# Performance work log

Measured on AMD Instinct MI355X. Metric: run time of the kernel, lower is better.

## Reference

```python
import jax, jax.numpy as jnp
import numpy as np

TOKENS = 8192
MODEL_DIM = 4096
PROMPT_DIM = 64
NUM_EXPERTS = 8
TOP_K = 2
EPS = float(np.finfo(np.float32).eps)


def setup_inputs() -> dict:
    key = jax.random.key(0)
    k1, k2, k3 = jax.random.split(key, 3)
    x = jax.random.normal(k1, (TOKENS, MODEL_DIM), dtype=jnp.float32)
    prompt = jax.random.normal(k2, (TOKENS, PROMPT_DIM), dtype=jnp.float32)
    # gate linear: Linear(model_dim + prompt_dim, num_experts, bias=True)
    W = jax.random.normal(k3, (MODEL_DIM + PROMPT_DIM, NUM_EXPERTS), dtype=jnp.float32) * 0.02
    b = jnp.zeros((NUM_EXPERTS,), dtype=jnp.float32)
    return {"x": x, "prompt": prompt, "W": W, "b": b}


def reference(x, prompt, W, b):
    # eval path: no jitter, no noise (self.training is False)
    logits = jnp.concatenate([x, prompt], axis=-1) @ W + b          # [T, E]
    _, topk_idx = jax.lax.top_k(logits, TOP_K)                      # [T, K]
    masks = jax.nn.one_hot(topk_idx, NUM_EXPERTS, dtype=jnp.float32)  # [T, K, E]
    gates = jax.nn.softmax(logits, axis=-1)                         # [T, E]
    gates_s = jnp.einsum("te,tke->tk", gates, masks)               # masked gather-sum
    if TOP_K > 1:
        denom = jnp.maximum(gates_s.sum(axis=-1, keepdims=True), EPS)
        gates_s = gates_s / denom
    # masks[:, i] == masks_se[i], gates_s[:, i] == gates_s[i] in the torch code
    return masks, gates_s
```

## Files before the change

### kernel.cpp

```cpp
#include <hip/hip_runtime.h>
#include <math.h>

#define NE 8
#define KDIM 4096
#define PDIM 64
#define WROWS (KDIM + PDIM)
#define EPS_F32 1.1920929e-07f
#define NCHUNK 16
#define DEPTH 3

typedef float f4 __attribute__((ext_vector_type(4)));

__global__ __launch_bounds__(256)
void transpose_w(const float* __restrict__ W, float* __restrict__ Wt) {
    const int k = blockIdx.x * 256 + threadIdx.x;
    if (k < WROWS) {
        float v[NE];
#pragma unroll
        for (int e = 0; e < NE; ++e) v[e] = W[(size_t)k * NE + e];
#pragma unroll
        for (int e = 0; e < NE; ++e) Wt[(size_t)e * WROWS + k] = v[e];
    }
}

__global__ __launch_bounds__(64, 2)
void topk_gate(const float* __restrict__ x,
               const float* __restrict__ prompt,
               const float* __restrict__ Wt,
               const float* __restrict__ b,
               float* __restrict__ out,
               int tokens)
{
    const int lane  = threadIdx.x;
    const int tbase = blockIdx.x * 4;
    const int klane = lane * 4;

    float acc[4][NE];
#pragma unroll
    for (int t = 0; t < 4; ++t)
#pragma unroll
        for (int e = 0; e < NE; ++e) acc[t][e] = 0.f;

    f4 xb[DEPTH][4];
    f4 wb[DEPTH][NE];

    auto load_chunk = [&](int c, int s) {
        const int k = c * 256 + klane;
#pragma unroll
        for (int t = 0; t < 4; ++t)
            xb[s][t] = __builtin_nontemporal_load(
                (const f4*)(x + (size_t)(tbase + t) * KDIM + k));
#pragma unroll
        for (int e = 0; e < NE; ++e)
            wb[s][e] = *(const f4*)(Wt + (size_t)e * WROWS + k);
    };

    load_chunk(0, 0);
    load_chunk(1, 1);

#pragma unroll
    for (int c = 0; c < NCHUNK; ++c) {
        if (c + 2 < NCHUNK) load_chunk(c + 2, (c + 2) % DEPTH);
        const int s = c % DEPTH;
#pragma unroll
        for (int t = 0; t < 4; ++t)
#pragma unroll
            for (int e = 0; e < NE; ++e) {
                acc[t][e] = fmaf(xb[s][t].x, wb[s][e].x, acc[t][e]);
                acc[t][e] = fmaf(xb[s][t].y, wb[s][e].y, acc[t][e]);
                acc[t][e] = fmaf(xb[s][t].z, wb[s][e].z, acc[t][e]);
                acc[t][e] = fmaf(xb[s][t].w, wb[s][e].w, acc[t][e]);
            }
    }

    if (lane < 16) {
        const int k = lane * 4;
        f4 pv[4];
#pragma unroll
        for (int t = 0; t < 4; ++t)
            pv[t] = *(const f4*)(prompt + (size_t)(tbase + t) * PDIM + k);
        f4 wv[NE];
#pragma unroll
        for (int e = 0; e < NE; ++e)
            wv[e] = *(const f4*)(Wt + (size_t)e * WROWS + KDIM + k);
#pragma unroll
        for (int t = 0; t < 4; ++t)
#pragma unroll
            for (int e = 0; e < NE; ++e) {
                acc[t][e] = fmaf(pv[t].x, wv[e].x, acc[t][e]);
                acc[t][e] = fmaf(pv[t].y, wv[e].y, acc[t][e]);
                acc[t][e] = fmaf(pv[t].z, wv[e].z, acc[t][e]);
                acc[t][e] = fmaf(pv[t].w, wv[e].w, acc[t][e]);
            }
    }

#pragma unroll
    for (int t = 0; t < 4; ++t)
#pragma unroll
        for (int e = 0; e < NE; ++e) {
            float v = acc[t][e];
#pragma unroll
            for (int off = 32; off >= 1; off >>= 1)
                v += __shfl_xor(v, off, 64);
            acc[t][e] = v;
        }

    const int tt = lane >> 4;
    const int kk = (lane >> 3) & 1;
    const int ee = lane & 7;

    float lg[NE];
#pragma unroll
    for (int e = 0; e < NE; ++e) {
        float v = acc[0][e];
        if (tt == 1) v = acc[1][e];
        if (tt == 2) v = acc[2][e];
        if (tt == 3) v = acc[3][e];
        lg[e] = v + b[e];
    }

    float v0 = lg[0]; int i0 = 0;
#pragma unroll
    for (int e = 1; e < NE; ++e)
        if (lg[e] > v0) { v0 = lg[e]; i0 = e; }
    float v1 = (i0 == 0) ? lg[1] : lg[0];
    int   i1 = (i0 == 0) ? 1 : 0;
#pragma unroll
    for (int e = 0; e < NE; ++e)
        if (e != i0 && lg[e] > v1) { v1 = lg[e]; i1 = e; }

    float s = 0.f;
#pragma unroll
    for (int e = 0; e < NE; ++e) s += __expf(lg[e] - v0);
    const float g0 = 1.0f / s;
    const float g1 = __expf(v1 - v0) / s;
    const float denom = fmaxf(g0 + g1, EPS_F32);

    const int sel = kk ? i1 : i0;
    const int t_global = tbase + tt;
    out[(size_t)t_global * 16 + kk * 8 + ee] = (ee == sel) ? 1.0f : 0.0f;

    if ((lane & 15) < 2) {
        const float g = (ee == 0) ? (g0 / denom) : (g1 / denom);
        out[(size_t)tokens * 16 + (size_t)t_global * 2 + ee] = g;
    }
}

extern "C" void kernel_launch(void* const* d_in, const int* in_sizes, int n_in,
                              void* d_out, int out_size, void* d_ws, size_t ws_size,
                              hipStream_t stream) {
    const float* x      = (const float*)d_in[0];
    const float* prompt = (const float*)d_in[1];
    const float* W      = (const float*)d_in[2];
    const float* b      = (const float*)d_in[3];
    float* out          = (float*)d_out;
    float* Wt           = (float*)d_ws;

    const int tokens = in_sizes[0] / KDIM;

    hipLaunchKernelGGL(transpose_w, dim3((WROWS + 255) / 256), dim3(256), 0, stream,
                       W, Wt);
    hipLaunchKernelGGL(topk_gate, dim3(tokens / 4), dim3(64), 0, stream,
                       x, prompt, Wt, b, out, tokens);
}
```

Before: 209.1 us.

## Split K into quarters with LDS-staged weights and separate top-k epilogue

```diff
diff --git a/kernel.cpp b/kernel.cpp
--- a/kernel.cpp
+++ b/kernel.cpp
@@ -4,36 +4,52 @@
 #define NE 8
 #define KDIM 4096
 #define PDIM 64
-#define WROWS (KDIM + PDIM)
+#define NQ 4
+#define QK (KDIM / NQ)
+#define TPB 16
+#define LROW (QK + 16)
 #define EPS_F32 1.1920929e-07f
-#define NCHUNK 16
-#define DEPTH 3
 
 typedef float f4 __attribute__((ext_vector_type(4)));
 
-__global__ __launch_bounds__(256)
-void transpose_w(const float* __restrict__ W, float* __restrict__ Wt) {
-    const int k = blockIdx.x * 256 + threadIdx.x;
-    if (k < WROWS) {
-        float v[NE];
+__global__ __launch_bounds__(256, 3)
+void gate_partial(const float* __restrict__ x,
+                  const float* __restrict__ prompt,
+                  const float* __restrict__ W,
+                  float* __restrict__ partials,
+                  int tokens)
+{
+    const int tid   = threadIdx.x;
+    const int lane  = tid & 63;
+    const int wave  = tid >> 6;
+    const int group = blockIdx.x >> 2;
+    const int q     = blockIdx.x & 3;
+    const int tbase = group * TPB + wave * 4;
+    const int k0    = q * QK;
+
+    __shared__ float lds_w[NE][LROW];
+
+    f4 xv[4][4];
 #pragma unroll
-        for (int e = 0; e < NE; ++e) v[e] = W[(size_t)k * NE + e];
+    for (int c = 0; c < 4; ++c)
 #pragma unroll
-        for (int e = 0; e < NE; ++e) Wt[(size_t)e * WROWS + k] = v[e];
+        for (int t = 0; t < 4; ++t)
+            xv[c][t] = __builtin_nontemporal_load(
+                (const f4*)(x + (size_t)(tbase + t) * KDIM + k0 + c * 256 + lane * 4));
+
+    const float* Wq = W + (size_t)k0 * NE;
+#pragma unroll
+    for (int it = 0; it < 8; ++it) {
+        const int m  = it * 256 + tid;
+        const f4 v   = *(const f4*)(Wq + 4 * m);
+        const int kl = m >> 1;
+        const int e0 = (m & 1) * 4;
+        lds_w[e0 + 0][kl] = v.x;
+        lds_w[e0 + 1][kl] = v.y;
+        lds_w[e0 + 2][kl] = v.z;
+        lds_w[e0 + 3][kl] = v.w;
     }
-}
-
-__global__ __launch_bounds__(64, 2)
-void topk_gate(const float* __restrict__ x,
-               const float* __restrict__ prompt,
-               const float* __restrict__ Wt,
-               const float* __restrict__ b,
-               float* __restrict__ out,
-               int tokens)
-{
-    const int lane  = threadIdx.x;
-    const int tbase = blockIdx.x * 4;
-    const int klane = lane * 4;
+    __syncthreads();
 
     float acc[4][NE];
 #pragma unroll
@@ -41,57 +57,50 @@
 #pragma unroll
         for (int e = 0; e < NE; ++e) acc[t][e] = 0.f;
 
-    f4 xb[DEPTH][4];
-    f4 wb[DEPTH][NE];
-
-    auto load_chunk = [&](int c, int s) {
-        const int k = c * 256 + klane;
 #pragma unroll
-        for (int t = 0; t < 4; ++t)
-            xb[s][t] = __builtin_nontemporal_load(
-                (const f4*)(x + (size_t)(tbase + t) * KDIM + k));
+    for (int c = 0; c < 4; ++c) {
+        f4 wv[NE];
 #pragma unroll
         for (int e = 0; e < NE; ++e)
-            wb[s][e] = *(const f4*)(Wt + (size_t)e * WROWS + k);
-    };
-
-    load_chunk(0, 0);
-    load_chunk(1, 1);
-
-#pragma unroll
-    for (int c = 0; c < NCHUNK; ++c) {
-        if (c + 2 < NCHUNK) load_chunk(c + 2, (c + 2) % DEPTH);
-        const int s = c % DEPTH;
+            wv[e] = *(const f4*)(&lds_w[e][c * 256 + lane * 4]);
 #pragma unroll
         for (int t = 0; t < 4; ++t)
 #pragma unroll
             for (int e = 0; e < NE; ++e) {
-                acc[t][e] = fmaf(xb[s][t].x, wb[s][e].x, acc[t][e]);
-                acc[t][e] = fmaf(xb[s][t].y, wb[s][e].y, acc[t][e]);
-                acc[t][e] = fmaf(xb[s][t].z, wb[s][e].z, acc[t][e]);
-                acc[t][e] = fmaf(xb[s][t].w, wb[s][e].w, acc[t][e]);
+                acc[t][e] = fmaf(xv[c][t].x, wv[e].x, acc[t][e]);
+                acc[t][e] = fmaf(xv[c][t].y, wv[e].y, acc[t][e]);
+                acc[t][e] = fmaf(xv[c][t].z, wv[e].z, acc[t][e]);
+                acc[t][e] = fmaf(xv[c][t].w, wv[e].w, acc[t][e]);
             }
     }
 
-    if (lane < 16) {
+    if (q == 3 && lane < 16) {
         const int k = lane * 4;
         f4 pv[4];
 #pragma unroll
         for (int t = 0; t < 4; ++t)
             pv[t] = *(const f4*)(prompt + (size_t)(tbase + t) * PDIM + k);
-        f4 wv[NE];
+        f4 wlo[4], whi[4];
 #pragma unroll
-        for (int e = 0; e < NE; ++e)
-            wv[e] = *(const f4*)(Wt + (size_t)e * WROWS + KDIM + k);
+        for (int j = 0; j < 4; ++j) {
+            wlo[j] = *(const f4*)(W + (size_t)(KDIM + k + j) * NE);
+            whi[j] = *(const f4*)(W + (size_t)(KDIM + k + j) * NE + 4);
+        }
 #pragma unroll
-        for (int t = 0; t < 4; ++t)
+        for (int t = 0; t < 4; ++t) {
+            const float* a = (const float*)&pv[t];
 #pragma unroll
-            for (int e = 0; e < NE; ++e) {
-                acc[t][e] = fmaf(pv[t].x, wv[e].x, acc[t][e]);
-                acc[t][e] = fmaf(pv[t].y, wv[e].y, acc[t][e]);
-                acc[t][e] = fmaf(pv[t].z, wv[e].z, acc[t][e]);
-                acc[t][e] = fmaf(pv[t].w, wv[e].w, acc[t][e]);
+            for (int j = 0; j < 4; ++j) {
+                acc[t][0] = fmaf(a[j], wlo[j].x, acc[t][0]);
+                acc[t][1] = fmaf(a[j], wlo[j].y, acc[t][1]);
+                acc[t][2] = fmaf(a[j], wlo[j].z, acc[t][2]);
+                acc[t][3] = fmaf(a[j], wlo[j].w, acc[t][3]);
+                acc[t][4] = fmaf(a[j], whi[j].x, acc[t][4]);
+                acc[t][5] = fmaf(a[j], whi[j].y, acc[t][5]);
+                acc[t][6] = fmaf(a[j], whi[j].z, acc[t][6]);
+                acc[t][7] = fmaf(a[j], whi[j].w, acc[t][7]);
             }
+        }
     }
 
 #pragma unroll
@@ -105,18 +114,38 @@
             acc[t][e] = v;
         }
 
+    if (lane < 32) {
+        const int t4 = lane >> 3;
+        const int e  = lane & 7;
+        partials[((size_t)q * tokens + tbase + t4) * NE + e] = acc[t4][e];
+    }
+}
+
+__global__ __launch_bounds__(256)
+void gate_epilogue(const float* __restrict__ partials,
+                   const float* __restrict__ b,
+                   float* __restrict__ out,
+                   int tokens)
+{
+    const int tid   = threadIdx.x;
+    const int lane  = tid & 63;
+    const int wave  = tid >> 6;
+    const int tbase = blockIdx.x * TPB + wave * 4;
+
     const int tt = lane >> 4;
     const int kk = (lane >> 3) & 1;
     const int ee = lane & 7;
+    const int tg = tbase + tt;
 
     float lg[NE];
 #pragma unroll
-    for (int e = 0; e < NE; ++e) {
-        float v = acc[0][e];
-        if (tt == 1) v = acc[1][e];
-        if (tt == 2) v = acc[2][e];
-        if (tt == 3) v = acc[3][e];
-        lg[e] = v + b[e];
+    for (int e = 0; e < NE; ++e) lg[e] = b[e];
+#pragma unroll
+    for (int qq = 0; qq < NQ; ++qq) {
+        const f4 lo = *(const f4*)(partials + ((size_t)qq * tokens + tg) * NE);
+        const f4 hi = *(const f4*)(partials + ((size_t)qq * tokens + tg) * NE + 4);
+        lg[0] += lo.x; lg[1] += lo.y; lg[2] += lo.z; lg[3] += lo.w;
+        lg[4] += hi.x; lg[5] += hi.y; lg[6] += hi.z; lg[7] += hi.w;
     }
 
     float v0 = lg[0]; int i0 = 0;
@@ -137,12 +166,11 @@
     const float denom = fmaxf(g0 + g1, EPS_F32);
 
     const int sel = kk ? i1 : i0;
-    const int t_global = tbase + tt;
-    out[(size_t)t_global * 16 + kk * 8 + ee] = (ee == sel) ? 1.0f : 0.0f;
+    out[(size_t)tg * 16 + kk * 8 + ee] = (ee == sel) ? 1.0f : 0.0f;
 
     if ((lane & 15) < 2) {
         const float g = (ee == 0) ? (g0 / denom) : (g1 / denom);
-        out[(size_t)tokens * 16 + (size_t)t_global * 2 + ee] = g;
+        out[(size_t)tokens * 16 + (size_t)tg * 2 + ee] = g;
     }
 }
 
@@ -154,12 +182,12 @@
     const float* W      = (const float*)d_in[2];
     const float* b      = (const float*)d_in[3];
     float* out          = (float*)d_out;
-    float* Wt           = (float*)d_ws;
+    float* partials     = (float*)d_ws;
 
     const int tokens = in_sizes[0] / KDIM;
 
-    hipLaunchKernelGGL(transpose_w, dim3((WROWS + 255) / 256), dim3(256), 0, stream,
-                       W, Wt);
-    hipLaunchKernelGGL(topk_gate, dim3(tokens / 4), dim3(64), 0, stream,
-                       x, prompt, Wt, b, out, tokens);
+    hipLaunchKernelGGL(gate_partial, dim3((tokens / TPB) * NQ), dim3(256), 0, stream,
+                       x, prompt, W, partials, tokens);
+    hipLaunchKernelGGL(gate_epilogue, dim3(tokens / TPB), dim3(256), 0, stream,
+                       partials, b, out, tokens);
 }
```

Result: slower. 222.0 us (+6.2%).

## Map one token per wavefront with 256-thread blocks to raise occupancy

Applied to the files above, without the earlier changes.

```diff
diff --git a/kernel.cpp b/kernel.cpp
--- a/kernel.cpp
+++ b/kernel.cpp
@@ -7,7 +7,6 @@
 #define WROWS (KDIM + PDIM)
 #define EPS_F32 1.1920929e-07f
 #define NCHUNK 16
-#define DEPTH 3
 
 typedef float f4 __attribute__((ext_vector_type(4)));
 
@@ -23,7 +22,7 @@
     }
 }
 
-__global__ __launch_bounds__(64, 2)
+__global__ __launch_bounds__(256, 8)
 void topk_gate(const float* __restrict__ x,
                const float* __restrict__ prompt,
                const float* __restrict__ Wt,
@@ -31,93 +30,78 @@
                float* __restrict__ out,
                int tokens)
 {
-    const int lane  = threadIdx.x;
-    const int tbase = blockIdx.x * 4;
+    const int lane = threadIdx.x & 63;
+    const int wave = threadIdx.x >> 6;
+    const int tg   = blockIdx.x * 4 + wave;
     const int klane = lane * 4;
 
-    float acc[4][NE];
+    const float* xrow = x + (size_t)tg * KDIM + klane;
+
+    float acc[NE];
 #pragma unroll
-    for (int t = 0; t < 4; ++t)
-#pragma unroll
-        for (int e = 0; e < NE; ++e) acc[t][e] = 0.f;
+    for (int e = 0; e < NE; ++e) acc[e] = 0.f;
 
-    f4 xb[DEPTH][4];
-    f4 wb[DEPTH][NE];
-
-    auto load_chunk = [&](int c, int s) {
-        const int k = c * 256 + klane;
-#pragma unroll
-        for (int t = 0; t < 4; ++t)
-            xb[s][t] = __builtin_nontemporal_load(
-                (const f4*)(x + (size_t)(tbase + t) * KDIM + k));
-#pragma unroll
-        for (int e = 0; e < NE; ++e)
-            wb[s][e] = *(const f4*)(Wt + (size_t)e * WROWS + k);
-    };
-
-    load_chunk(0, 0);
-    load_chunk(1, 1);
+    f4 xb[2];
+    xb[0] = __builtin_nontemporal_load((const f4*)(xrow));
+    xb[1] = __builtin_nontemporal_load((const f4*)(xrow + 256));
 
 #pragma unroll
     for (int c = 0; c < NCHUNK; ++c) {
-        if (c + 2 < NCHUNK) load_chunk(c + 2, (c + 2) % DEPTH);
-        const int s = c % DEPTH;
+        const int cur = c & 1;
+        const f4 xv = xb[cur];
+        if (c + 2 < NCHUNK)
+            xb[cur] = __builtin_nontemporal_load((const f4*)(xrow + (c + 2) * 256));
+
+        const int k = c * 256 + klane;
 #pragma unroll
-        for (int t = 0; t < 4; ++t)
+        for (int eh = 0; eh < 2; ++eh) {
+            f4 wv[4];
 #pragma unroll
-            for (int e = 0; e < NE; ++e) {
-                acc[t][e] = fmaf(xb[s][t].x, wb[s][e].x, acc[t][e]);
-                acc[t][e] = fmaf(xb[s][t].y, wb[s][e].y, acc[t][e]);
-                acc[t][e] = fmaf(xb[s][t].z, wb[s][e].z, acc[t][e]);
-                acc[t][e] = fmaf(xb[s][t].w, wb[s][e].w, acc[t][e]);
+            for (int j = 0; j < 4; ++j)
+                wv[j] = *(const f4*)(Wt + (size_t)(eh * 4 + j) * WROWS + k);
+#pragma unroll
+            for (int j = 0; j < 4; ++j) {
+                const int e = eh * 4 + j;
+                acc[e] = fmaf(xv.x, wv[j].x, acc[e]);
+                acc[e] = fmaf(xv.y, wv[j].y, acc[e]);
+                acc[e] = fmaf(xv.z, wv[j].z, acc[e]);
+                acc[e] = fmaf(xv.w, wv[j].w, acc[e]);
             }
+        }
     }
 
     if (lane < 16) {
         const int k = lane * 4;
-        f4 pv[4];
+        const f4 pv = *(const f4*)(prompt + (size_t)tg * PDIM + k);
 #pragma unroll
-        for (int t = 0; t < 4; ++t)
-            pv[t] = *(const f4*)(prompt + (size_t)(tbase + t) * PDIM + k);
-        f4 wv[NE];
+        for (int eh = 0; eh < 2; ++eh) {
+            f4 wv[4];
 #pragma unroll
-        for (int e = 0; e < NE; ++e)
-            wv[e] = *(const f4*)(Wt + (size_t)e * WROWS + KDIM + k);
+            for (int j = 0; j < 4; ++j)
+                wv[j] = *(const f4*)(Wt + (size_t)(eh * 4 + j) * WROWS + KDIM + k);
 #pragma unroll
-        for (int t = 0; t < 4; ++t)
-#pragma unroll
-            for (int e = 0; e < NE; ++e) {
-                acc[t][e] = fmaf(pv[t].x, wv[e].x, acc[t][e]);
-                acc[t][e] = fmaf(pv[t].y, wv[e].y, acc[t][e]);
-                acc[t][e] = fmaf(pv[t].z, wv[e].z, acc[t][e]);
-                acc[t][e] = fmaf(pv[t].w, wv[e].w, acc[t][e]);
+            for (int j = 0; j < 4; ++j) {
+                const int e = eh * 4 + j;
+                acc[e] = fmaf(pv.x, wv[j].x, acc[e]);
+                acc[e] = fmaf(pv.y, wv[j].y, acc[e]);
+                acc[e] = fmaf(pv.z, wv[j].z, acc[e]);
+                acc[e] = fmaf(pv.w, wv[j].w, acc[e]);
             }
+        }
     }
 
 #pragma unroll
-    for (int t = 0; t < 4; ++t)
+    for (int e = 0; e < NE; ++e) {
+        float v = acc[e];
 #pragma unroll
-        for (int e = 0; e < NE; ++e) {
-            float v = acc[t][e];
-#pragma unroll
-            for (int off = 32; off >= 1; off >>= 1)
-                v += __shfl_xor(v, off, 64);
-            acc[t][e] = v;
-        }
-
-    const int tt = lane >> 4;
-    const int kk = (lane >> 3) & 1;
-    const int ee = lane & 7;
+        for (int off = 32; off >= 1; off >>= 1)
+            v += __shfl_xor(v, off, 64);
+        acc[e] = v;
+    }
 
     float lg[NE];
 #pragma unroll
-    for (int e = 0; e < NE; ++e) {
-        float v = acc[0][e];
-        if (tt == 1) v = acc[1][e];
-        if (tt == 2) v = acc[2][e];
-        if (tt == 3) v = acc[3][e];
-        lg[e] = v + b[e];
-    }
+    for (int e = 0; e < NE; ++e) lg[e] = acc[e] + b[e];
 
     float v0 = lg[0]; int i0 = 0;
 #pragma unroll
@@ -136,14 +120,16 @@
     const float g1 = __expf(v1 - v0) / s;
     const float denom = fmaxf(g0 + g1, EPS_F32);
 
-    const int sel = kk ? i1 : i0;
-    const int t_global = tbase + tt;
-    out[(size_t)t_global * 16 + kk * 8 + ee] = (ee == sel) ? 1.0f : 0.0f;
-
-    if ((lane & 15) < 2) {
-        const float g = (ee == 0) ? (g0 / denom) : (g1 / denom);
-        out[(size_t)tokens * 16 + (size_t)t_global * 2 + ee] = g;
+    if (lane < 16) {
+        const int kk  = lane >> 3;
+        const int ee  = lane & 7;
+        const int sel = kk ? i1 : i0;
+        out[(size_t)tg * 16 + lane] = (ee == sel) ? 1.0f : 0.0f;
     }
+    if (lane == 0)
+        out[(size_t)tokens * 16 + (size_t)tg * 2 + 0] = g0 / denom;
+    if (lane == 8)
+        out[(size_t)tokens * 16 + (size_t)tg * 2 + 1] = g1 / denom;
 }
 
 extern "C" void kernel_launch(void* const* d_in, const int* in_sizes, int n_in,
@@ -160,6 +146,6 @@
 
     hipLaunchKernelGGL(transpose_w, dim3((WROWS + 255) / 256), dim3(256), 0, stream,
                        W, Wt);
-    hipLaunchKernelGGL(topk_gate, dim3(tokens / 4), dim3(64), 0, stream,
+    hipLaunchKernelGGL(topk_gate, dim3(tokens / 4), dim3(256), 0, stream,
                        x, prompt, Wt, b, out, tokens);
 }
```

After: 235.9 us. 1.13x slower.
